# Performance work log

Measured on AMD Instinct MI355X. Metric: run time of the kernel, lower is better.

Reference implementation:

```python
import jax, jax.numpy as jnp
import numpy as np
import math

B = 16; L = 1024; CIN = 3; COUT = 1; D = 128; K = 16; DEPTH = 4
EPS = 1e-5; GRID_RANGE = 1.0


def _haar_basis(L):
    # Orthonormal Haar wavelet basis, rows of V (L, L). L must be power of 2.
    V = np.zeros((L, L), dtype=np.float64)
    V[0, :] = 1.0 / math.sqrt(L)
    r, s = 1, 1
    while s < L and r < L:
        block = 2 * s
        amp = 1.0 / math.sqrt(block)
        for j in range(L // block):
            st = j * block
            V[r, st:st + s] = amp
            V[r, st + s:st + block] = -amp
            r += 1
            if r >= L:
                break
        s *= 2
    return V


def _phi_f(L, k):
    # rFFT of top-k Haar basis rows, complex64 (matches build_stu_basis_rfft)
    V = _haar_basis(L)
    return jnp.asarray(np.fft.rfft(V, axis=-1)[:k].astype(np.complex64))


def setup_inputs() -> dict:
    key = jax.random.key(0)
    ks = jax.random.split(key, 8)

    def rn(k, shape, scale):
        return jax.random.normal(k, shape, dtype=jnp.float32) * scale

    return {
        "x": jax.random.normal(ks[0], (B, CIN, L), dtype=jnp.float32),
        "lift_w": rn(ks[1], (D, CIN + 1), 1.0 / math.sqrt(CIN + 1)),  # conv1x1 weight
        "lift_b": jnp.zeros((D,), jnp.float32),
        "Phi_f": _phi_f(L, K),                                        # (K, L//2+1) complex64 buffer
        "theta": rn(ks[2], (DEPTH, K, D, D), 1.0 / math.sqrt(D)),
        "ln_g": jnp.ones((DEPTH, D), jnp.float32),
        "ln_b": jnp.zeros((DEPTH, D), jnp.float32),
        "fc1_w": rn(ks[3], (DEPTH, 2 * D, D), 1.0 / math.sqrt(D)),
        "fc1_b": jnp.zeros((DEPTH, 2 * D), jnp.float32),
        "fc2_w": rn(ks[4], (DEPTH, D, 2 * D), 1.0 / math.sqrt(2 * D)),
        "fc2_b": jnp.zeros((DEPTH, D), jnp.float32),
        "head_w": rn(ks[5], (COUT, D), 1.0 / math.sqrt(D)),
        "head_b": jnp.zeros((COUT,), jnp.float32),
    }


def _forward(x, lift_w, lift_b, Phi_f, theta, ln_g, ln_b,
             fc1_w, fc1_b, fc2_w, fc2_b, head_w, head_b):
    # add_grid: append linspace coord channel -> (B, CIN+1, L)
    coords = jnp.linspace(0.0, GRID_RANGE, L, dtype=x.dtype)
    coords = jnp.broadcast_to(coords, (x.shape[0], 1, L))
    xg = jnp.concatenate([x, coords], axis=1)

    # LocalLift1D with kernel_size=1 == pointwise linear over channels
    h = jnp.einsum('bcl,dc->bdl', xg, lift_w) + lift_b[None, :, None]

    Phic = jnp.conj(Phi_f)  # (K, Lr)
    for i in range(DEPTH):
        # LayerNorm over channel dim (torch LN on transposed (B,L,D))
        mu = jnp.mean(h, axis=1, keepdims=True)
        var = jnp.var(h, axis=1, keepdims=True)
        z = (h - mu) / jnp.sqrt(var + EPS) * ln_g[i][None, :, None] + ln_b[i][None, :, None]

        Xf = jnp.fft.rfft(z, axis=-1)                       # (B, D, Lr)
        Uf = Xf[:, :, None, :] * Phic[None, None, :, :]     # (B, D, K, Lr)
        U = jnp.fft.irfft(Uf, n=L, axis=-1)                 # (B, D, K, L)

        # fused einsum('bdln,lhd->bhln') + sum over l(=k)
        S = jnp.einsum('bdkn,khd->bhn', U, theta[i])        # (B, D, L)

        # pointwise MLP (conv1x1 -> GELU -> conv1x1), residual
        H1 = jax.nn.gelu(jnp.einsum('bdl,hd->bhl', S, fc1_w[i]) + fc1_b[i][None, :, None],
                         approximate=False)
        h = h + jnp.einsum('bhl,dh->bdl', H1, fc2_w[i]) + fc2_b[i][None, :, None]

    # head: conv1x1 lifting_dim -> out_dim
    return jnp.einsum('bdl,od->bol', h, head_w) + head_b[None, :, None]


def reference(x, lift_w, lift_b, Phi_f, theta, ln_g, ln_b,
              fc1_w, fc1_b, fc2_w, fc2_b, head_w, head_b):
    return _forward(x, lift_w, lift_b, Phi_f, theta, ln_g, ln_b,
                    fc1_w, fc1_b, fc2_w, fc2_b, head_w, head_b)
```

## Files before the change

kernel.cpp:

```cpp
#include <hip/hip_runtime.h>
#include <math.h>

#define BB 16
#define LL 1024
#define DD 128
#define BL (BB*LL)
#define NDEPTH 4
#define EPSF 1e-5f

typedef unsigned short u16;
typedef short bf16x8 __attribute__((ext_vector_type(8)));
typedef short bf16x4 __attribute__((ext_vector_type(4)));
typedef float f32x4 __attribute__((ext_vector_type(4)));

static __device__ __forceinline__ u16 f2bf(float x) {
    unsigned u = __float_as_uint(x);
    u = u + 0x7fffu + ((u >> 16) & 1u);
    return (u16)(u >> 16);
}
static __device__ __forceinline__ float bf2f(short v) {
    return __uint_as_float(((unsigned)(unsigned short)v) << 16);
}

#define DZ_B  0
#define S_B   15360
#define H1_B  23552
#define ZS_B  39936
#define C_B   40448
#define RST_B 40960
#define MRS_B 41088
#define LDS_TOT 41216

#define N_TH (4*15*16384)
#define N_W1 (4*32768)
#define N_W2 (4*32768)
#define N_TH0 (4*16384)
__global__ __launch_bounds__(256) void cvt_kernel(const float* __restrict__ theta,
        const float* __restrict__ fc1w, const float* __restrict__ fc2w,
        u16* __restrict__ thf, u16* __restrict__ w1f, u16* __restrict__ w2f,
        u16* __restrict__ th0f) {
    int o = blockIdx.x * 256 + threadIdx.x;
    if (o < N_TH) {
        int j = o & 7, ln = (o >> 3) & 63, c = (o >> 9) & 3, f = (o >> 11) & 7;
        int slab = o >> 14;
        int layer = slab / 15, kk = slab - layer * 15;
        int h = f * 16 + (ln & 15), d = 32 * c + 8 * (ln >> 4) + j;
        thf[o] = f2bf(theta[(((size_t)layer * 16 + kk + 1) * 128 + h) * 128 + d]);
    } else if (o < N_TH + N_W1) {
        int o2 = o - N_TH;
        int j = o2 & 7, ln = (o2 >> 3) & 63, c = (o2 >> 9) & 3, f = (o2 >> 11) & 15;
        int layer = o2 >> 15;
        int m = f * 16 + (ln & 15), d = 32 * c + 8 * (ln >> 4) + j;
        w1f[o2] = f2bf(fc1w[(size_t)layer * 32768 + m * 128 + d]);
    } else if (o < N_TH + N_W1 + N_W2) {
        int o2 = o - (N_TH + N_W1);
        int j = o2 & 7, ln = (o2 >> 3) & 63, c = (o2 >> 9) & 7, f = (o2 >> 12) & 7;
        int layer = o2 >> 15;
        int d = f * 16 + (ln & 15), m = 32 * c + 8 * (ln >> 4) + j;
        w2f[o2] = f2bf(fc2w[(size_t)layer * 32768 + d * 256 + m]);
    } else if (o < N_TH + N_W1 + N_W2 + N_TH0) {
        int o2 = o - (N_TH + N_W1 + N_W2);
        int layer = o2 >> 14, idx = o2 & 16383;
        th0f[o2] = f2bf(theta[(size_t)layer * 262144 + idx]);
    }
}

__global__ __launch_bounds__(512) void prep0_kernel(const float* __restrict__ x,
        const float* __restrict__ lw, const float* __restrict__ lb,
        float* __restrict__ H, float2* __restrict__ stats,
        float* __restrict__ P1p, float* __restrict__ P2p) {
    __shared__ char lds[16384 + 256];
    float* rst = (float*)(lds + 16384);
    float* mrs = (float*)(lds + 16384 + 128);
    int b = blockIdx.y, nblk = blockIdx.x, t0 = nblk * 32, tid = threadIdx.x;

    #pragma unroll
    for (int it = 0; it < 2; ++it) {
        int idx = it * 512 + tid;
        int r = idx >> 5, d0 = (idx & 31) * 4;
        int l = t0 + r;
        float x0 = x[(size_t)b * 3072 + l];
        float x1 = x[(size_t)b * 3072 + 1024 + l];
        float x2 = x[(size_t)b * 3072 + 2048 + l];
        float coord = (float)l * (1.0f / 1023.0f);
        f32x4 hv;
        #pragma unroll
        for (int q = 0; q < 4; ++q) {
            int d = d0 + q;
            float4 w = *(const float4*)(lw + d * 4);
            hv[q] = lb[d] + w.x * x0 + w.y * x1 + w.z * x2 + w.w * coord;
        }
        *(f32x4*)(H + ((size_t)b * 1024 + l) * 128 + d0) = hv;
        int byte = r * 512 + ((d0 * 4) ^ ((r & 7) << 4));
        *(f32x4*)(lds + byte) = hv;
    }
    __syncthreads();
    {
        int t = tid >> 4, q = tid & 15;
        float s = 0.f, sq = 0.f;
        #pragma unroll
        for (int dd = 0; dd < 8; dd += 4) {
            int d = q * 8 + dd;
            int byte = t * 512 + ((d * 4) ^ ((t & 7) << 4));
            f32x4 v = *(const f32x4*)(lds + byte);
            s += v[0] + v[1] + v[2] + v[3];
            sq += v[0]*v[0] + v[1]*v[1] + v[2]*v[2] + v[3]*v[3];
        }
        #pragma unroll
        for (int o = 1; o < 16; o <<= 1) {
            s += __shfl_xor(s, o, 64); sq += __shfl_xor(sq, o, 64);
        }
        if (q == 0) {
            float mu = s * (1.f / 128.f);
            float var = sq * (1.f / 128.f) - mu * mu;
            float rs = rsqrtf(var + EPSF);
            stats[(size_t)b * 1024 + t0 + t] = make_float2(mu, rs);
            rst[t] = rs; mrs[t] = mu * rs;
        }
    }
    __syncthreads();
    if (tid < 128) {
        float s = 0.f;
        #pragma unroll 8
        for (int t = 0; t < 32; ++t) {
            int byte = t * 512 + ((tid * 4) ^ ((t & 7) << 4));
            s += *(const float*)(lds + byte) * rst[t];
        }
        P1p[((size_t)b * 32 + nblk) * 128 + tid] = s;
    } else if (tid == 128) {
        float s = 0.f;
        for (int t = 0; t < 32; ++t) s += mrs[t];
        P2p[b * 32 + nblk] = s;
    }
}

template<int LAST>
__global__ __launch_bounds__(512, 4) void mega_kernel(
        const float* __restrict__ Hin, const float2* __restrict__ stin,
        const float* __restrict__ lng, const float* __restrict__ lnb,
        const u16* __restrict__ thf, const u16* __restrict__ th0f,
        const u16* __restrict__ w1f, const float* __restrict__ b1,
        const u16* __restrict__ w2f, const float* __restrict__ b2,
        float* __restrict__ Hout, float2* __restrict__ stout,
        const float* __restrict__ P1in, const float* __restrict__ P2in,
        float* __restrict__ P1out, float* __restrict__ P2out,
        const float* __restrict__ hwp, const float* __restrict__ hbp,
        float* __restrict__ out) {
    __shared__ char lds[LDS_TOT];
    int b = blockIdx.y, nblk = blockIdx.x, n0 = nblk * 32, tid = threadIdx.x;
    const float inv_s2 = 0.70710678118654752f;

    const float* Hb = Hin + (size_t)b * 1024 * 128;
    const float2* stb = stin + (size_t)b * 1024;
    for (int c = tid; c < 60 * 16; c += 512) {
        int r = c >> 4, d0 = (c & 15) * 8;
        int gr = (n0 + r) & 1023, g1 = (n0 + r + 1) & 1023;
        const float* ha = Hb + (size_t)gr * 128 + d0;
        const float* hc = Hb + (size_t)g1 * 128 + d0;
        float2 sa = stb[gr], sb = stb[g1];
        u16 tmp[8];
        #pragma unroll
        for (int j = 0; j < 8; ++j) {
            float za = (ha[j] - sa.x) * sa.y;
            float zc = (hc[j] - sb.x) * sb.y;
            tmp[j] = f2bf((za - zc) * inv_s2 * lng[d0 + j]);
        }
        int byte = r * 256 + ((d0 * 2) ^ ((r & 7) << 4));
        *(bf16x8*)(lds + byte) = *(bf16x8*)tmp;
    }
    if (tid < 128) {
        float s = 0.f;
        #pragma unroll 8
        for (int j = 0; j < 32; ++j) s += P1in[((size_t)b * 32 + j) * 128 + tid];
        float p2 = 0.f;
        #pragma unroll 8
        for (int j = 0; j < 32; ++j) p2 += P2in[b * 32 + j];
        ((float*)(lds + ZS_B))[tid] = lng[tid] * (s - p2) + 1024.0f * lnb[tid];
    }
    __syncthreads();

    int wave = tid >> 6, lane = tid & 63;
    int lm = lane & 15, lk = (lane >> 4) * 8;
    f32x4 zero4 = {0.f, 0.f, 0.f, 0.f};

    {
        int h = tid >> 2, q = tid & 3;
        const u16* th0 = th0f + h * 128 + q * 32;
        const float* zs = (const float*)(lds + ZS_B) + q * 32;
        float acc = 0.f;
        #pragma unroll
        for (int c = 0; c < 4; ++c) {
            bf16x8 tv = *(const bf16x8*)(th0 + c * 8);
            #pragma unroll
            for (int j = 0; j < 8; ++j) acc += bf2f(tv[j]) * zs[c * 8 + j];
        }
        acc += __shfl_xor(acc, 1, 64);
        acc += __shfl_xor(acc, 2, 64);
        if (q == 0) ((float*)(lds + C_B))[h] = acc * (1.0f / 32.0f);
    }
    __syncthreads();

    f32x4 accS[2] = {zero4, zero4};
    {
        const u16* thl = thf + (size_t)lane * 8 + (size_t)wave * 2048;
        bf16x8 bufA[4], bufB[4];
        #pragma unroll
        for (int c4 = 0; c4 < 4; ++c4)
            bufA[c4] = *(const bf16x8*)(thl + c4 * 512);
        #pragma unroll
        for (int kp = 0; kp < 7; ++kp) {
            int kk = kp * 2;
            #pragma unroll
            for (int c4 = 0; c4 < 4; ++c4)
                bufB[c4] = *(const bf16x8*)(thl + (size_t)(kk + 1) * 16384 + c4 * 512);
            #pragma unroll
            for (int c4 = 0; c4 < 4; ++c4) {
                #pragma unroll
                for (int nt = 0; nt < 2; ++nt) {
                    int trow = nt * 16 + lm + 2 * kk;
                    int byte = trow * 256 + (((c4 * 32 + lk) * 2) ^ ((trow & 7) << 4));
                    bf16x8 bfr = *(const bf16x8*)(lds + byte);
                    accS[nt] = __builtin_amdgcn_mfma_f32_16x16x32_bf16(bufA[c4], bfr, accS[nt], 0, 0, 0);
                }
            }
            #pragma unroll
            for (int c4 = 0; c4 < 4; ++c4)
                bufA[c4] = *(const bf16x8*)(thl + (size_t)(kk + 2) * 16384 + c4 * 512);
            #pragma unroll
            for (int c4 = 0; c4 < 4; ++c4) {
                #pragma unroll
                for (int nt = 0; nt < 2; ++nt) {
                    int trow = nt * 16 + lm + 2 * (kk + 1);
                    int byte = trow * 256 + (((c4 * 32 + lk) * 2) ^ ((trow & 7) << 4));
                    bf16x8 bfr = *(const bf16x8*)(lds + byte);
                    accS[nt] = __builtin_amdgcn_mfma_f32_16x16x32_bf16(bufB[c4], bfr, accS[nt], 0, 0, 0);
                }
            }
        }
        #pragma unroll
        for (int c4 = 0; c4 < 4; ++c4) {
            #pragma unroll
            for (int nt = 0; nt < 2; ++nt) {
                int trow = nt * 16 + lm + 28;
                int byte = trow * 256 + (((c4 * 32 + lk) * 2) ^ ((trow & 7) << 4));
                bf16x8 bfr = *(const bf16x8*)(lds + byte);
                accS[nt] = __builtin_amdgcn_mfma_f32_16x16x32_bf16(bufA[c4], bfr, accS[nt], 0, 0, 0);
            }
        }
    }

    {
        int h0 = wave * 16 + (lane >> 4) * 4;
        f32x4 cv = *(const f32x4*)(lds + C_B + h0 * 4);
        #pragma unroll
        for (int nt = 0; nt < 2; ++nt) {
            int tl = nt * 16 + lm;
            u16 o[4];
            #pragma unroll
            for (int r = 0; r < 4; ++r) o[r] = f2bf(accS[nt][r] + cv[r]);
            int byte = S_B + tl * 256 + ((h0 * 2) ^ ((tl & 7) << 4));
            *(bf16x4*)(lds + byte) = *(bf16x4*)o;
        }
    }
    __syncthreads();

    {
        f32x4 acc1[2][2];
        #pragma unroll
        for (int mt = 0; mt < 2; ++mt)
            #pragma unroll
            for (int nt = 0; nt < 2; ++nt) acc1[mt][nt] = zero4;
        const u16* w1l = w1f + (size_t)lane * 8;
        #pragma unroll
        for (int c4 = 0; c4 < 4; ++c4) {
            bf16x8 afr[2], bfr[2];
            #pragma unroll
            for (int mt = 0; mt < 2; ++mt)
                afr[mt] = *(const bf16x8*)(w1l + ((size_t)((wave * 2 + mt) * 4 + c4) << 9));
            #pragma unroll
            for (int nt = 0; nt < 2; ++nt) {
                int tl = nt * 16 + lm;
                int byte = S_B + tl * 256 + (((c4 * 32 + lk) * 2) ^ ((tl & 7) << 4));
                bfr[nt] = *(const bf16x8*)(lds + byte);
            }
            #pragma unroll
            for (int mt = 0; mt < 2; ++mt)
                #pragma unroll
                for (int nt = 0; nt < 2; ++nt)
                    acc1[mt][nt] = __builtin_amdgcn_mfma_f32_16x16x32_bf16(
                        afr[mt], bfr[nt], acc1[mt][nt], 0, 0, 0);
        }
        #pragma unroll
        for (int mt = 0; mt < 2; ++mt) {
            int mo = wave * 32 + mt * 16 + (lane >> 4) * 4;
            f32x4 bb4 = *(const f32x4*)(b1 + mo);
            #pragma unroll
            for (int nt = 0; nt < 2; ++nt) {
                int tl = nt * 16 + lm;
                u16 o[4];
                #pragma unroll
                for (int r = 0; r < 4; ++r) {
                    float xv = acc1[mt][nt][r] + bb4[r];
                    o[r] = f2bf(0.5f * xv * (1.0f + erff(xv * 0.70710678118654752f)));
                }
                int byte = H1_B + tl * 512 + ((mo * 2) ^ ((tl & 7) << 4));
                *(bf16x4*)(lds + byte) = *(bf16x4*)o;
            }
        }
    }
    __syncthreads();

    f32x4 acc2[2] = {zero4, zero4};
    {
        const u16* w2l = w2f + (size_t)lane * 8;
        #pragma unroll
        for (int c8 = 0; c8 < 8; ++c8) {
            bf16x8 afr = *(const bf16x8*)(w2l + ((size_t)(wave * 8 + c8) << 9));
            #pragma unroll
            for (int nt = 0; nt < 2; ++nt) {
                int tl = nt * 16 + lm;
                int byte = H1_B + tl * 512 + (((c8 * 32 + lk) * 2) ^ ((tl & 7) << 4));
                bf16x8 bfr = *(const bf16x8*)(lds + byte);
                acc2[nt] = __builtin_amdgcn_mfma_f32_16x16x32_bf16(afr, bfr, acc2[nt], 0, 0, 0);
            }
        }
    }
    __syncthreads();

    {
        int dbase = wave * 16 + (lane >> 4) * 4;
        #pragma unroll
        for (int nt = 0; nt < 2; ++nt) {
            int tl = nt * 16 + lm;
            int byte = H1_B + tl * 512 + ((dbase * 4) ^ ((tl & 7) << 4));
            *(f32x4*)(lds + byte) = acc2[nt];
        }
    }
    __syncthreads();

    {
        const float* Hrow = Hin + ((size_t)b * 1024 + n0) * 128;
        float* Horow = Hout + ((size_t)b * 1024 + n0) * 128;
        #pragma unroll
        for (int it = 0; it < 2; ++it) {
            int idx = it * 512 + tid;
            int r = idx >> 5, d0 = (idx & 31) * 4;
            int byte = H1_B + r * 512 + ((d0 * 4) ^ ((r & 7) << 4));
            f32x4 v = *(const f32x4*)(lds + byte);
            f32x4 bb = *(const f32x4*)(b2 + d0);
            f32x4 hv = *(const f32x4*)(Hrow + (size_t)r * 128 + d0);
            hv = hv + v + bb;
            if (LAST) {
                f32x4 wv = *(const f32x4*)(hwp + d0);
                float s = hv[0]*wv[0] + hv[1]*wv[1] + hv[2]*wv[2] + hv[3]*wv[3];
                #pragma unroll
                for (int o = 1; o < 32; o <<= 1) s += __shfl_xor(s, o, 64);
                if ((lane & 31) == 0) out[(size_t)b * 1024 + n0 + r] = s + hbp[0];
            } else {
                *(f32x4*)(Horow + (size_t)r * 128 + d0) = hv;
                *(f32x4*)(lds + byte) = hv;
            }
        }
    }
    if (!LAST) {
        __syncthreads();
        float* rst = (float*)(lds + RST_B);
        float* mrs = (float*)(lds + MRS_B);
        {
            int t = tid >> 4, q = tid & 15;
            float s = 0.f, sq = 0.f;
            #pragma unroll
            for (int dd = 0; dd < 8; dd += 4) {
                int d = q * 8 + dd;
                int byte = H1_B + t * 512 + ((d * 4) ^ ((t & 7) << 4));
                f32x4 v = *(const f32x4*)(lds + byte);
                s += v[0] + v[1] + v[2] + v[3];
                sq += v[0]*v[0] + v[1]*v[1] + v[2]*v[2] + v[3]*v[3];
            }
            #pragma unroll
            for (int o = 1; o < 16; o <<= 1) {
                s += __shfl_xor(s, o, 64); sq += __shfl_xor(sq, o, 64);
            }
            if (q == 0) {
                float mu = s * (1.f / 128.f);
                float var = sq * (1.f / 128.f) - mu * mu;
                float rs = rsqrtf(var + EPSF);
                stout[(size_t)b * 1024 + n0 + t] = make_float2(mu, rs);
                rst[t] = rs; mrs[t] = mu * rs;
            }
        }
        __syncthreads();
        if (tid < 128) {
            float s = 0.f;
            #pragma unroll 8
            for (int t = 0; t < 32; ++t) {
                int byte = H1_B + t * 512 + ((tid * 4) ^ ((t & 7) << 4));
                s += *(const float*)(lds + byte) * rst[t];
            }
            P1out[((size_t)b * 32 + nblk) * 128 + tid] = s;
        } else if (tid == 128) {
            float s = 0.f;
            for (int t = 0; t < 32; ++t) s += mrs[t];
            P2out[b * 32 + nblk] = s;
        }
    }
}

extern "C" void kernel_launch(void* const* d_in, const int* in_sizes, int n_in,
                              void* d_out, int out_size, void* d_ws, size_t ws_size,
                              hipStream_t stream) {
    const float* x     = (const float*)d_in[0];
    const float* lw    = (const float*)d_in[1];
    const float* lb    = (const float*)d_in[2];
    const float* theta = (const float*)d_in[4];
    const float* ln_g  = (const float*)d_in[5];
    const float* ln_b  = (const float*)d_in[6];
    const float* fc1w  = (const float*)d_in[7];
    const float* fc1b  = (const float*)d_in[8];
    const float* fc2w  = (const float*)d_in[9];
    const float* fc2b  = (const float*)d_in[10];
    const float* hw    = (const float*)d_in[11];
    const float* hb    = (const float*)d_in[12];

    float* ws = (float*)d_ws;
    float* H_A = ws;
    float* H_B = H_A + (size_t)BL * DD;
    float2* st_A = (float2*)(H_B + (size_t)BL * DD);
    float2* st_B = st_A + BL;
    float* P1A = (float*)(st_B + BL);
    float* P1B = P1A + 16 * 32 * 128;
    float* P2A = P1B + 16 * 32 * 128;
    float* P2B = P2A + 512;
    u16* thf  = (u16*)(P2B + 512);
    u16* w1f  = thf + N_TH;
    u16* w2f  = w1f + N_W1;
    u16* th0f = w2f + N_W2;

    cvt_kernel<<<(N_TH + N_W1 + N_W2 + N_TH0) / 256, 256, 0, stream>>>(
        theta, fc1w, fc2w, thf, w1f, w2f, th0f);
    prep0_kernel<<<dim3(32, 16), 512, 0, stream>>>(x, lw, lb, H_A, st_A, P1A, P2A);

    float* Hi = H_A; float* Ho = H_B;
    float2* sti = st_A; float2* sto = st_B;
    float* p1i = P1A; float* p1o = P1B;
    float* p2i = P2A; float* p2o = P2B;
    for (int i = 0; i < NDEPTH; ++i) {
        if (i < NDEPTH - 1) {
            mega_kernel<0><<<dim3(32, 16), 512, 0, stream>>>(
                Hi, sti, ln_g + i * 128, ln_b + i * 128,
                thf + (size_t)i * 15 * 16384, th0f + (size_t)i * 16384,
                w1f + (size_t)i * 32768, fc1b + i * 256,
                w2f + (size_t)i * 32768, fc2b + i * 128,
                Ho, sto, p1i, p2i, p1o, p2o, hw, hb, (float*)d_out);
        } else {
            mega_kernel<1><<<dim3(32, 16), 512, 0, stream>>>(
                Hi, sti, ln_g + i * 128, ln_b + i * 128,
                thf + (size_t)i * 15 * 16384, th0f + (size_t)i * 16384,
                w1f + (size_t)i * 32768, fc1b + i * 256,
                w2f + (size_t)i * 32768, fc2b + i * 128,
                Ho, sto, p1i, p2i, p1o, p2o, hw, hb, (float*)d_out);
        }
        float* t;
        t = Hi; Hi = Ho; Ho = t;
        float2* ts = sti; sti = sto; sto = ts;
        t = p1i; p1i = p1o; p1o = t;
        t = p2i; p2i = p2o; p2o = t;
    }
}
```

Baseline: 148.2 us.

## Fold LN gain into theta, hoist global loads, fast GELU, flatten theta loop

```diff
diff --git a/kernel.cpp b/kernel.cpp
--- a/kernel.cpp
+++ b/kernel.cpp
@@ -20,6 +20,17 @@
 }
 static __device__ __forceinline__ float bf2f(short v) {
     return __uint_as_float(((unsigned)(unsigned short)v) << 16);
+}
+static __device__ __forceinline__ float gelu_f(float x) {
+    float u = x * 0.70710678118654752f;
+    float au = fabsf(u);
+    float t = __builtin_amdgcn_rcpf(1.0f + 0.3275911f * au);
+    float poly = ((((1.061405429f * t - 1.453152027f) * t + 1.421413741f) * t
+                   - 0.284496736f) * t + 0.254829592f) * t;
+    float e = __expf(-u * u);
+    float erfv = 1.0f - poly * e;
+    erfv = copysignf(erfv, u);
+    return 0.5f * x * (1.0f + erfv);
 }
 
 #define DZ_B  0
@@ -37,6 +48,7 @@
 #define N_TH0 (4*16384)
 __global__ __launch_bounds__(256) void cvt_kernel(const float* __restrict__ theta,
         const float* __restrict__ fc1w, const float* __restrict__ fc2w,
+        const float* __restrict__ ln_g,
         u16* __restrict__ thf, u16* __restrict__ w1f, u16* __restrict__ w2f,
         u16* __restrict__ th0f) {
     int o = blockIdx.x * 256 + threadIdx.x;
@@ -45,7 +57,9 @@
         int slab = o >> 14;
         int layer = slab / 15, kk = slab - layer * 15;
         int h = f * 16 + (ln & 15), d = 32 * c + 8 * (ln >> 4) + j;
-        thf[o] = f2bf(theta[(((size_t)layer * 16 + kk + 1) * 128 + h) * 128 + d]);
+        float v = theta[(((size_t)layer * 16 + kk + 1) * 128 + h) * 128 + d];
+        v *= ln_g[layer * 128 + d] * 0.70710678118654752f;
+        thf[o] = f2bf(v);
     } else if (o < N_TH + N_W1) {
         int o2 = o - N_TH;
         int j = o2 & 7, ln = (o2 >> 3) & 63, c = (o2 >> 9) & 3, f = (o2 >> 11) & 15;
@@ -148,7 +162,21 @@
         float* __restrict__ out) {
     __shared__ char lds[LDS_TOT];
     int b = blockIdx.y, nblk = blockIdx.x, n0 = nblk * 32, tid = threadIdx.x;
-    const float inv_s2 = 0.70710678118654752f;
+
+    float zacc = 0.f, p2 = 0.f;
+    if (tid < 128) {
+        #pragma unroll 8
+        for (int j = 0; j < 32; ++j) zacc += P1in[((size_t)b * 32 + j) * 128 + tid];
+        #pragma unroll 8
+        for (int j = 0; j < 32; ++j) p2 += P2in[b * 32 + j];
+    }
+    bf16x8 tv[4];
+    {
+        int h = tid >> 2, q = tid & 3;
+        const u16* th0 = th0f + h * 128 + q * 32;
+        #pragma unroll
+        for (int c = 0; c < 4; ++c) tv[c] = *(const bf16x8*)(th0 + c * 8);
+    }
 
     const float* Hb = Hin + (size_t)b * 1024 * 128;
     const float2* stb = stin + (size_t)b * 1024;
@@ -163,20 +191,13 @@
         for (int j = 0; j < 8; ++j) {
             float za = (ha[j] - sa.x) * sa.y;
             float zc = (hc[j] - sb.x) * sb.y;
-            tmp[j] = f2bf((za - zc) * inv_s2 * lng[d0 + j]);
+            tmp[j] = f2bf(za - zc);
         }
         int byte = r * 256 + ((d0 * 2) ^ ((r & 7) << 4));
         *(bf16x8*)(lds + byte) = *(bf16x8*)tmp;
     }
-    if (tid < 128) {
-        float s = 0.f;
-        #pragma unroll 8
-        for (int j = 0; j < 32; ++j) s += P1in[((size_t)b * 32 + j) * 128 + tid];
-        float p2 = 0.f;
-        #pragma unroll 8
-        for (int j = 0; j < 32; ++j) p2 += P2in[b * 32 + j];
-        ((float*)(lds + ZS_B))[tid] = lng[tid] * (s - p2) + 1024.0f * lnb[tid];
-    }
+    if (tid < 128)
+        ((float*)(lds + ZS_B))[tid] = lng[tid] * (zacc - p2) + 1024.0f * lnb[tid];
     __syncthreads();
 
     int wave = tid >> 6, lane = tid & 63;
@@ -185,15 +206,12 @@
 
     {
         int h = tid >> 2, q = tid & 3;
-        const u16* th0 = th0f + h * 128 + q * 32;
         const float* zs = (const float*)(lds + ZS_B) + q * 32;
         float acc = 0.f;
         #pragma unroll
-        for (int c = 0; c < 4; ++c) {
-            bf16x8 tv = *(const bf16x8*)(th0 + c * 8);
-            #pragma unroll
-            for (int j = 0; j < 8; ++j) acc += bf2f(tv[j]) * zs[c * 8 + j];
-        }
+        for (int c = 0; c < 4; ++c)
+            #pragma unroll
+            for (int j = 0; j < 8; ++j) acc += bf2f(tv[c][j]) * zs[c * 8 + j];
         acc += __shfl_xor(acc, 1, 64);
         acc += __shfl_xor(acc, 2, 64);
         if (q == 0) ((float*)(lds + C_B))[h] = acc * (1.0f / 32.0f);
@@ -202,49 +220,17 @@
 
     f32x4 accS[2] = {zero4, zero4};
     {
-        const u16* thl = thf + (size_t)lane * 8 + (size_t)wave * 2048;
-        bf16x8 bufA[4], bufB[4];
-        #pragma unroll
-        for (int c4 = 0; c4 < 4; ++c4)
-            bufA[c4] = *(const bf16x8*)(thl + c4 * 512);
-        #pragma unroll
-        for (int kp = 0; kp < 7; ++kp) {
-            int kk = kp * 2;
-            #pragma unroll
-            for (int c4 = 0; c4 < 4; ++c4)
-                bufB[c4] = *(const bf16x8*)(thl + (size_t)(kk + 1) * 16384 + c4 * 512);
-            #pragma unroll
-            for (int c4 = 0; c4 < 4; ++c4) {
-                #pragma unroll
-                for (int nt = 0; nt < 2; ++nt) {
-                    int trow = nt * 16 + lm + 2 * kk;
-                    int byte = trow * 256 + (((c4 * 32 + lk) * 2) ^ ((trow & 7) << 4));
-                    bf16x8 bfr = *(const bf16x8*)(lds + byte);
-                    accS[nt] = __builtin_amdgcn_mfma_f32_16x16x32_bf16(bufA[c4], bfr, accS[nt], 0, 0, 0);
-                }
-            }
-            #pragma unroll
-            for (int c4 = 0; c4 < 4; ++c4)
-                bufA[c4] = *(const bf16x8*)(thl + (size_t)(kk + 2) * 16384 + c4 * 512);
-            #pragma unroll
-            for (int c4 = 0; c4 < 4; ++c4) {
-                #pragma unroll
-                for (int nt = 0; nt < 2; ++nt) {
-                    int trow = nt * 16 + lm + 2 * (kk + 1);
-                    int byte = trow * 256 + (((c4 * 32 + lk) * 2) ^ ((trow & 7) << 4));
-                    bf16x8 bfr = *(const bf16x8*)(lds + byte);
-                    accS[nt] = __builtin_amdgcn_mfma_f32_16x16x32_bf16(bufB[c4], bfr, accS[nt], 0, 0, 0);
-                }
-            }
-        }
-        #pragma unroll
-        for (int c4 = 0; c4 < 4; ++c4) {
+        const u16* thl = thf + (size_t)lane * 8;
+        #pragma unroll
+        for (int it = 0; it < 60; ++it) {
+            int kk = it >> 2, c4 = it & 3;
+            bf16x8 afr = *(const bf16x8*)(thl + ((size_t)((kk * 8 + wave) * 4 + c4) << 9));
             #pragma unroll
             for (int nt = 0; nt < 2; ++nt) {
-                int trow = nt * 16 + lm + 28;
+                int trow = nt * 16 + lm + 2 * kk;
                 int byte = trow * 256 + (((c4 * 32 + lk) * 2) ^ ((trow & 7) << 4));
                 bf16x8 bfr = *(const bf16x8*)(lds + byte);
-                accS[nt] = __builtin_amdgcn_mfma_f32_16x16x32_bf16(bufA[c4], bfr, accS[nt], 0, 0, 0);
+                accS[nt] = __builtin_amdgcn_mfma_f32_16x16x32_bf16(afr, bfr, accS[nt], 0, 0, 0);
             }
         }
     }
@@ -299,10 +285,8 @@
                 int tl = nt * 16 + lm;
                 u16 o[4];
                 #pragma unroll
-                for (int r = 0; r < 4; ++r) {
-                    float xv = acc1[mt][nt][r] + bb4[r];
-                    o[r] = f2bf(0.5f * xv * (1.0f + erff(xv * 0.70710678118654752f)));
-                }
+                for (int r = 0; r < 4; ++r)
+                    o[r] = f2bf(gelu_f(acc1[mt][nt][r] + bb4[r]));
                 int byte = H1_B + tl * 512 + ((mo * 2) ^ ((tl & 7) << 4));
                 *(bf16x4*)(lds + byte) = *(bf16x4*)o;
             }
@@ -437,7 +421,7 @@
     u16* th0f = w2f + N_W2;
 
     cvt_kernel<<<(N_TH + N_W1 + N_W2 + N_TH0) / 256, 256, 0, stream>>>(
-        theta, fc1w, fc2w, thf, w1f, w2f, th0f);
+        theta, fc1w, fc2w, ln_g, thf, w1f, w2f, th0f);
     prep0_kernel<<<dim3(32, 16), 512, 0, stream>>>(x, lw, lb, H_A, st_A, P1A, P2A);
 
     float* Hi = H_A; float* Ho = H_B;
```

Result: slower. 169.2 us (+14.2%).
